# Optimization experiments

Measured on AMD Instinct MI355X. Metric: run time of the kernel, lower is better.

Reference implementation:

```python
import jax, jax.numpy as jnp
import numpy as np
import math

EPS = 1.1920929e-07  # torch default rms_norm eps = finfo(float32).eps

def rms_norm(x):
    return x * jax.lax.rsqrt(jnp.mean(x * x, axis=-1, keepdims=True) + EPS)

def setup_inputs() -> dict:
    key = jax.random.key(0)
    k1, k2, k3, k4 = jax.random.split(key, 4)
    B, T, D = 2, 4096, 2048
    H = 16
    L = (T - 1).bit_length()  # 12
    scale = 0.02
    return {
        "x": jax.random.normal(k1, (B, T, D), dtype=jnp.float32),
        "W_tok": jax.random.normal(k2, (D, D), dtype=jnp.float32) * scale,
        "W_lvl": jax.random.normal(k3, (L * H, D), dtype=jnp.float32) * scale,
        "W_out": jax.random.normal(k4, (D, D), dtype=jnp.float32) * scale,
        "num_heads": H,
    }

def reference(x, W_tok, W_lvl, W_out, num_heads):
    B, T, D = x.shape
    H = num_heads
    Dh = D // H
    L = W_lvl.shape[0] // H  # max_lvls
    inv_sqrt2 = 1.0 / math.sqrt(2.0)

    theta = rms_norm(jnp.einsum('btd,ed->bte', x, W_tok)).reshape(B, T, H, Dh)
    phi = rms_norm(jnp.einsum('btd,ed->bte', x, W_lvl)).reshape(B, T, L, H)

    for l in range(L):  # log-depth butterfly over fixed L levels
        step = 1 << l
        phi_l = phi[:, :, l][..., None]  # [B,T,H,1]
        if step < T:
            theta_prev = jnp.concatenate(
                [jnp.zeros_like(theta[:, :step]), theta[:, :-step]], axis=1)
        else:
            theta_prev = jnp.zeros_like(theta)
        theta = (jnp.cos(phi_l) * theta + jnp.sin(phi_l) * theta_prev) * inv_sqrt2

    y = jnp.einsum('btd,ed->bte', theta.reshape(B, T, D), W_out)
    return y
```

## Files before the change

### kernel.cpp

```cpp
#include <hip/hip_runtime.h>
#include <cstdint>

typedef unsigned short u16;
typedef short bh8 __attribute__((ext_vector_type(8)));
typedef float f32x4 __attribute__((ext_vector_type(4)));

#define EPSF 1.1920929e-07f
#define INV_SQRT2 0.70710678118654752440f

static constexpr size_t OFF_XB   = 0;
static constexpr size_t OFF_WCAT = 33554432;
static constexpr size_t OFF_WOUT = OFF_WCAT + 9437184;
static constexpr size_t OFF_THBF = OFF_WOUT + 8388608;
static constexpr size_t OFF_PHI  = OFF_THBF + 33554432;
static constexpr size_t OFF_TRA  = OFF_PHI + 6291456;
static constexpr size_t OFF_TRB  = OFF_TRA + 6291456;

__device__ __forceinline__ uint32_t f2bf_rne(float f) {
  uint32_t u = __float_as_uint(f);
  u += 0x7fffu + ((u >> 16) & 1u);
  return u >> 16;
}

__device__ __forceinline__ void gload_lds16(const void* g, void* l) {
  __builtin_amdgcn_global_load_lds(
      (const __attribute__((address_space(1))) void*)g,
      (__attribute__((address_space(3))) void*)l, 16, 0, 0);
}

__global__ __launch_bounds__(256)
void cast_f32_bf16(const float* __restrict__ src, u16* __restrict__ dst, int n4) {
  int i = blockIdx.x * blockDim.x + threadIdx.x;
  int stride = gridDim.x * blockDim.x;
  for (; i < n4; i += stride) {
    float4 v = ((const float4*)src)[i];
    uint32_t a = __float_as_uint(v.x); a += 0x7fffu + ((a >> 16) & 1u);
    uint32_t b = __float_as_uint(v.y); b += 0x7fffu + ((b >> 16) & 1u);
    uint32_t c = __float_as_uint(v.z); c += 0x7fffu + ((c >> 16) & 1u);
    uint32_t d = __float_as_uint(v.w); d += 0x7fffu + ((d >> 16) & 1u);
    uint2 o;
    o.x = (a >> 16) | (b & 0xffff0000u);
    o.y = (c >> 16) | (d & 0xffff0000u);
    ((uint2*)dst)[i] = o;
  }
}

__global__ __launch_bounds__(256)
void zero_u16(u16* __restrict__ dst, int n) {
  int i = blockIdx.x * blockDim.x + threadIdx.x;
  int stride = gridDim.x * blockDim.x;
  for (; i < n; i += stride) dst[i] = 0;
}

template<int SPLIT>
__global__ __launch_bounds__(256)
void gemm_bt(const u16* __restrict__ A, const u16* __restrict__ B,
             float* __restrict__ C0, float* __restrict__ C1,
             int K, int ntiles) {
  __shared__ u16 As[128 * 64];
  __shared__ u16 Bs[128 * 64];
  const int tid  = threadIdx.x;
  const int w    = tid >> 6;
  const int lane = tid & 63;
  const int mt = blockIdx.x / ntiles, nt = blockIdx.x % ntiles;
  const int wm = (w >> 1) << 6, wn = (w & 1) << 6;
  const int Kb = K * 2;

  const char* Ab = (const char*)(A + (size_t)mt * 128 * K);
  const char* Bb = (const char*)(B + (size_t)nt * 128 * K);
  char* AsB = (char*)As;
  char* BsB = (char*)Bs;

  const int srow  = w * 8 + (lane >> 3);
  const int scolb = (lane & 7) << 4;

  f32x4 acc[4][4] = {};

  for (int kt = 0; kt < K; kt += 64) {
    #pragma unroll
    for (int i = 0; i < 4; ++i) {
      int row = i * 32 + srow;
      int src = scolb ^ ((row & 7) << 4);
      gload_lds16(Ab + (size_t)row * Kb + kt * 2 + src, AsB + i * 4096 + w * 1024);
      gload_lds16(Bb + (size_t)row * Kb + kt * 2 + src, BsB + i * 4096 + w * 1024);
    }
    __syncthreads();
    #pragma unroll
    for (int kk = 0; kk < 2; ++kk) {
      const int kbyte = kk * 64 + ((lane >> 4) << 4);
      bh8 af[4], bfr[4];
      #pragma unroll
      for (int m = 0; m < 4; ++m) {
        int ar = wm + m * 16 + (lane & 15);
        af[m] = *(const bh8*)(AsB + ar * 128 + (kbyte ^ ((ar & 7) << 4)));
        int br = wn + m * 16 + (lane & 15);
        bfr[m] = *(const bh8*)(BsB + br * 128 + (kbyte ^ ((br & 7) << 4)));
      }
      #pragma unroll
      for (int m = 0; m < 4; ++m)
        #pragma unroll
        for (int n = 0; n < 4; ++n)
          acc[m][n] = __builtin_amdgcn_mfma_f32_16x16x32_bf16(af[m], bfr[n], acc[m][n], 0, 0, 0);
    }
    __syncthreads();
  }

  const int crow0 = mt * 128 + wm + ((lane >> 4) << 2);
  const int ccol0 = nt * 128 + wn + (lane & 15);
  #pragma unroll
  for (int m = 0; m < 4; ++m) {
    #pragma unroll
    for (int n = 0; n < 4; ++n) {
      int gn = ccol0 + n * 16;
      #pragma unroll
      for (int r = 0; r < 4; ++r) {
        int gm = crow0 + m * 16 + r;
        if (SPLIT) {
          if (gn < 2048)      C0[(size_t)gm * 2048 + gn] = acc[m][n][r];
          else if (gn < 2240) C1[(size_t)gm * 192 + (gn - 2048)] = acc[m][n][r];
        } else {
          C0[(size_t)gm * 2048 + gn] = acc[m][n][r];
        }
      }
    }
  }
}

__global__ __launch_bounds__(256)
void rmsnorm_rows(float* __restrict__ th) {
  const int row = blockIdx.x;
  const int tid = threadIdx.x;
  float* p = th + (size_t)row * 2048;
  float4 a = ((const float4*)p)[tid];
  float4 b = ((const float4*)p)[tid + 256];
  float ss = a.x*a.x + a.y*a.y + a.z*a.z + a.w*a.w
           + b.x*b.x + b.y*b.y + b.z*b.z + b.w*b.w;
  #pragma unroll
  for (int o = 32; o > 0; o >>= 1) ss += __shfl_down(ss, o);
  __shared__ float red[4];
  if ((tid & 63) == 0) red[tid >> 6] = ss;
  __syncthreads();
  float tot = red[0] + red[1] + red[2] + red[3];
  float s = rsqrtf(tot * (1.0f / 2048.0f) + EPSF);
  a.x *= s; a.y *= s; a.z *= s; a.w *= s;
  b.x *= s; b.y *= s; b.z *= s; b.w *= s;
  ((float4*)p)[tid] = a;
  ((float4*)p)[tid + 256] = b;
}

__global__ __launch_bounds__(64)
void phi_pass(const float* __restrict__ phiraw,
              float* __restrict__ trigA, float* __restrict__ trigB) {
  const int row = blockIdx.x;
  const int tid = threadIdx.x;
  const float* pr = phiraw + (size_t)row * 192;
  float v0 = pr[tid], v1 = pr[tid + 64], v2 = pr[tid + 128];
  float ss = v0 * v0 + v1 * v1 + v2 * v2;
  #pragma unroll
  for (int o = 32; o > 0; o >>= 1) ss += __shfl_down(ss, o);
  ss = __shfl(ss, 0);
  const float sc = rsqrtf(ss * (1.0f / 192.0f) + EPSF);
  const int b = row >> 12, t = row & 4095;
  const int q = t >> 6, r = t & 63;
  float v[3] = {v0, v1, v2};
  #pragma unroll
  for (int j = 0; j < 3; ++j) {
    int e = j * 64 + tid;
    int l = e >> 4, h = e & 15;
    float ph = v[j] * sc;
    float sn, cs;
    sincosf(ph, &sn, &cs);
    if (l < 6) {
      size_t idx = ((size_t)((b * 16 + h) * 6 + l)) * 4096 + t;
      trigA[idx] = cs; trigA[idx + 786432] = sn;
    } else {
      size_t idx = ((size_t)((b * 16 + h) * 6 + (l - 6))) * 4096 + (size_t)(r * 64 + q);
      trigB[idx] = cs; trigB[idx + 786432] = sn;
    }
  }
}

__global__ __launch_bounds__(512)
void butterflyA(const float* __restrict__ in, u16* __restrict__ outb,
                const float* __restrict__ trigA) {
  __shared__ float L[512 * 32];
  const int tc = blockIdx.x, ec = blockIdx.y, b = blockIdx.z;
  const int tid = threadIdx.x;
  const int t0 = tc * 449;
  const int e0 = ec * 32;
  const int h = e0 >> 7;
  const int pr = tid >> 3;
  const int c4 = (tid & 7) << 2;

  #pragma unroll
  for (int s = 0; s < 8; ++s) {
    int p = pr + s * 64;
    int t = t0 - 63 + p;
    float4 v = make_float4(0.f, 0.f, 0.f, 0.f);
    if (t >= 0 && t < 4096)
      v = *(const float4*)&in[((size_t)(b * 4096 + t)) * 2048 + e0 + c4];
    *(float4*)&L[p * 32 + c4] = v;
  }
  __syncthreads();

  for (int l = 0; l < 6; ++l) {
    const int step = 1 << l;
    const float* cosT = trigA + ((size_t)((b * 16 + h) * 6 + l)) * 4096;
    const float* sinT = cosT + 786432;
    float4 nv[8];
    #pragma unroll
    for (int s = 0; s < 8; ++s) {
      int p = pr + s * 64;
      int t = t0 - 63 + p;
      float4 cur = *(const float4*)&L[p * 32 + c4];
      float4 prev = make_float4(0.f, 0.f, 0.f, 0.f);
      if (p >= step) prev = *(const float4*)&L[(p - step) * 32 + c4];
      float cs = 0.f, sn = 0.f;
      if (t >= 0 && t < 4096) { cs = cosT[t]; sn = sinT[t]; }
      nv[s].x = (cs * cur.x + sn * prev.x) * INV_SQRT2;
      nv[s].y = (cs * cur.y + sn * prev.y) * INV_SQRT2;
      nv[s].z = (cs * cur.z + sn * prev.z) * INV_SQRT2;
      nv[s].w = (cs * cur.w + sn * prev.w) * INV_SQRT2;
    }
    __syncthreads();
    #pragma unroll
    for (int s = 0; s < 8; ++s) {
      int p = pr + s * 64;
      *(float4*)&L[p * 32 + c4] = nv[s];
    }
    __syncthreads();
  }

  #pragma unroll
  for (int s = 0; s < 8; ++s) {
    int p = pr + s * 64;
    int t = t0 - 63 + p;
    if (p >= 63 && t < 4096) {
      float4 v = *(const float4*)&L[p * 32 + c4];
      uint32_t a = f2bf_rne(v.x), bb = f2bf_rne(v.y), c = f2bf_rne(v.z), d = f2bf_rne(v.w);
      uint2 o;
      o.x = a | (bb << 16);
      o.y = c | (d << 16);
      *(uint2*)&outb[((size_t)(b * 4096 + t)) * 2048 + e0 + c4] = o;
    }
  }
}

__global__ __launch_bounds__(256)
void butterflyB(const u16* __restrict__ in, u16* __restrict__ outb,
                const float* __restrict__ trigB) {
  __shared__ float L[64 * 128];
  const int r = blockIdx.x, h = blockIdx.y, b = blockIdx.z;
  const int tid = threadIdx.x;
  const int qr = tid >> 5;
  const int d4 = (tid & 31) << 2;

  #pragma unroll
  for (int s = 0; s < 8; ++s) {
    int q = qr + s * 8;
    int t = q * 64 + r;
    uint2 o = *(const uint2*)&in[((size_t)(b * 4096 + t)) * 2048 + h * 128 + d4];
    float4 v;
    v.x = __uint_as_float((o.x & 0xffffu) << 16);
    v.y = __uint_as_float(o.x & 0xffff0000u);
    v.z = __uint_as_float((o.y & 0xffffu) << 16);
    v.w = __uint_as_float(o.y & 0xffff0000u);
    *(float4*)&L[q * 128 + d4] = v;
  }
  __syncthreads();

  for (int l = 0; l < 6; ++l) {
    const int qs = 1 << l;
    const float* cosT = trigB + ((size_t)((b * 16 + h) * 6 + l)) * 4096 + r * 64;
    const float* sinT = cosT + 786432;
    float4 nv[8];
    #pragma unroll
    for (int s = 0; s < 8; ++s) {
      int q = qr + s * 8;
      float4 cur = *(const float4*)&L[q * 128 + d4];
      float4 prev = make_float4(0.f, 0.f, 0.f, 0.f);
      if (q >= qs) prev = *(const float4*)&L[(q - qs) * 128 + d4];
      float cs = cosT[q], sn = sinT[q];
      nv[s].x = (cs * cur.x + sn * prev.x) * INV_SQRT2;
      nv[s].y = (cs * cur.y + sn * prev.y) * INV_SQRT2;
      nv[s].z = (cs * cur.z + sn * prev.z) * INV_SQRT2;
      nv[s].w = (cs * cur.w + sn * prev.w) * INV_SQRT2;
    }
    __syncthreads();
    #pragma unroll
    for (int s = 0; s < 8; ++s) {
      int q = qr + s * 8;
      *(float4*)&L[q * 128 + d4] = nv[s];
    }
    __syncthreads();
  }

  #pragma unroll
  for (int s = 0; s < 8; ++s) {
    int q = qr + s * 8;
    int t = q * 64 + r;
    float4 v = *(const float4*)&L[q * 128 + d4];
    uint32_t a = f2bf_rne(v.x), bb = f2bf_rne(v.y), c = f2bf_rne(v.z), d = f2bf_rne(v.w);
    uint2 o;
    o.x = a | (bb << 16);
    o.y = c | (d << 16);
    *(uint2*)&outb[((size_t)(b * 4096 + t)) * 2048 + h * 128 + d4] = o;
  }
}

extern "C" void kernel_launch(void* const* d_in, const int* in_sizes, int n_in,
                              void* d_out, int out_size, void* d_ws, size_t ws_size,
                              hipStream_t stream) {
  const float* x    = (const float*)d_in[0];
  const float* Wtok = (const float*)d_in[1];
  const float* Wlvl = (const float*)d_in[2];
  const float* Wout = (const float*)d_in[3];

  char* ws = (char*)d_ws;
  u16*   xb     = (u16*)(ws + OFF_XB);
  u16*   wcat   = (u16*)(ws + OFF_WCAT);
  u16*   woutb  = (u16*)(ws + OFF_WOUT);
  u16*   thbfA  = (u16*)(ws + OFF_XB);
  u16*   thbfB  = (u16*)(ws + OFF_THBF);
  float* phiraw = (float*)(ws + OFF_PHI);
  float* trigA  = (float*)(ws + OFF_TRA);
  float* trigB  = (float*)(ws + OFF_TRB);
  float* out    = (float*)d_out;

  cast_f32_bf16<<<2048, 256, 0, stream>>>(x, xb, 4194304);
  cast_f32_bf16<<<1024, 256, 0, stream>>>(Wtok, wcat, 1048576);
  cast_f32_bf16<<<384, 256, 0, stream>>>(Wlvl, wcat + (size_t)2048 * 2048, 98304);
  zero_u16<<<128, 256, 0, stream>>>(wcat + (size_t)2240 * 2048, 131072);
  cast_f32_bf16<<<1024, 256, 0, stream>>>(Wout, woutb, 1048576);

  gemm_bt<1><<<64 * 18, 256, 0, stream>>>(xb, wcat, out, phiraw, 2048, 18);

  rmsnorm_rows<<<8192, 256, 0, stream>>>(out);

  phi_pass<<<8192, 64, 0, stream>>>(phiraw, trigA, trigB);

  butterflyA<<<dim3(10, 64, 2), 512, 0, stream>>>(out, thbfA, trigA);

  butterflyB<<<dim3(64, 16, 2), 256, 0, stream>>>(thbfA, thbfB, trigB);

  gemm_bt<0><<<64 * 16, 256, 0, stream>>>(thbfB, woutb, out, nullptr, 2048, 16);
}
```

Baseline: 461.9 us.

## Replace GEMMs with 256x256 triple-buffered kernel, fuse rmsnorm into epilogue, split-K phi

Replaces the 128x128 GEMM with a 256x256-tile, 512-thread kernel that triple-buffers LDS loads, raises MFMA priority and remaps workgroups in XCD-aware order. The first GEMM computes per-row sum-of-squares via atomics, so the separate rmsnorm pass is dropped and the scaling is applied when the butterfly loads. The small phi projection is computed as split-K tiles whose partials are summed in phi_pass, which now uses fast __sinf/__cosf and one unified trig layout. The aim is less memory traffic and better MFMA utilization, at the cost of atomics, reduced trig precision and greater register/LDS pressure.

```diff
diff --git a/kernel.cpp b/kernel.cpp
--- a/kernel.cpp
+++ b/kernel.cpp
@@ -7,14 +7,14 @@
 
 #define EPSF 1.1920929e-07f
 #define INV_SQRT2 0.70710678118654752440f
+#define SINOFF 1572864
 
 static constexpr size_t OFF_XB   = 0;
 static constexpr size_t OFF_WCAT = 33554432;
 static constexpr size_t OFF_WOUT = OFF_WCAT + 9437184;
 static constexpr size_t OFF_THBF = OFF_WOUT + 8388608;
-static constexpr size_t OFF_PHI  = OFF_THBF + 33554432;
-static constexpr size_t OFF_TRA  = OFF_PHI + 6291456;
-static constexpr size_t OFF_TRB  = OFF_TRA + 6291456;
+static constexpr size_t OFF_TRIG = OFF_THBF + 33554432;
+static constexpr size_t OFF_SSQ  = OFF_TRIG + 12582912;
 
 __device__ __forceinline__ uint32_t f2bf_rne(float f) {
   uint32_t u = __float_as_uint(f);
@@ -26,6 +26,12 @@
   __builtin_amdgcn_global_load_lds(
       (const __attribute__((address_space(1))) void*)g,
       (__attribute__((address_space(3))) void*)l, 16, 0, 0);
+}
+
+__global__ __launch_bounds__(256)
+void zero_f32(float4* __restrict__ p, int n4) {
+  int i = blockIdx.x * blockDim.x + threadIdx.x;
+  if (i < n4) p[i] = make_float4(0.f, 0.f, 0.f, 0.f);
 }
 
 __global__ __launch_bounds__(256)
@@ -45,144 +51,166 @@
   }
 }
 
-__global__ __launch_bounds__(256)
-void zero_u16(u16* __restrict__ dst, int n) {
-  int i = blockIdx.x * blockDim.x + threadIdx.x;
-  int stride = gridDim.x * blockDim.x;
-  for (; i < n; i += stride) dst[i] = 0;
-}
-
-template<int SPLIT>
-__global__ __launch_bounds__(256)
-void gemm_bt(const u16* __restrict__ A, const u16* __restrict__ B,
-             float* __restrict__ C0, float* __restrict__ C1,
-             int K, int ntiles) {
-  __shared__ u16 As[128 * 64];
-  __shared__ u16 Bs[128 * 64];
+template<int MODE>
+__global__ __launch_bounds__(512, 2)
+void gemm8(const u16* __restrict__ A, const u16* __restrict__ B,
+           float* __restrict__ C, float* __restrict__ phiq,
+           float* __restrict__ sumsq, int nwg) {
+  __shared__ __align__(16) char ldsb[98304];
   const int tid  = threadIdx.x;
   const int w    = tid >> 6;
   const int lane = tid & 63;
-  const int mt = blockIdx.x / ntiles, nt = blockIdx.x % ntiles;
-  const int wm = (w >> 1) << 6, wn = (w & 1) << 6;
-  const int Kb = K * 2;
-
-  const char* Ab = (const char*)(A + (size_t)mt * 128 * K);
-  const char* Bb = (const char*)(B + (size_t)nt * 128 * K);
-  char* AsB = (char*)As;
-  char* BsB = (char*)Bs;
-
-  const int srow  = w * 8 + (lane >> 3);
-  const int scolb = (lane & 7) << 4;
-
-  f32x4 acc[4][4] = {};
-
-  for (int kt = 0; kt < K; kt += 64) {
-    #pragma unroll
-    for (int i = 0; i < 4; ++i) {
-      int row = i * 32 + srow;
-      int src = scolb ^ ((row & 7) << 4);
-      gload_lds16(Ab + (size_t)row * Kb + kt * 2 + src, AsB + i * 4096 + w * 1024);
-      gload_lds16(Bb + (size_t)row * Kb + kt * 2 + src, BsB + i * 4096 + w * 1024);
-    }
-    __syncthreads();
-    #pragma unroll
-    for (int kk = 0; kk < 2; ++kk) {
-      const int kbyte = kk * 64 + ((lane >> 4) << 4);
-      bh8 af[4], bfr[4];
+  const int cpx = nwg >> 3;
+  const int wg  = ((int)blockIdx.x & 7) * cpx + ((int)blockIdx.x >> 3);
+
+  int mt, nt, t0, TT, kq = 0;
+  bool isphi = false;
+  if (MODE == 0) { mt = wg >> 3; nt = wg & 7; t0 = 0; TT = 64; }
+  else {
+    if (wg < 256) { mt = wg >> 3; nt = wg & 7; t0 = 0; TT = 64; }
+    else { int idx = wg - 256; mt = idx >> 2; kq = idx & 3; nt = 8; t0 = kq * 16; TT = 16; isphi = true; }
+  }
+  const int wr = w >> 2, wc = w & 3;
+
+  const char* Ab = (const char*)A + (size_t)mt * 256 * 4096;
+  const char* Bb = (const char*)B + (size_t)nt * 256 * 4096;
+
+  const int row0 = ((tid >> 6) << 4) + (tid & 15);
+  const int g16  = ((tid >> 4) & 3) << 4;
+  const char* sA0 = Ab + (size_t)row0 * 4096 + g16 + (size_t)t0 * 64;
+  const char* sA1 = sA0 + 128 * 4096;
+  const char* sB0 = Bb + (size_t)row0 * 4096 + g16 + (size_t)t0 * 64;
+  const char* sB1 = sB0 + 128 * 4096;
+  const int wB = w * 1024;
+  const int lo16 = lane * 16;
+
+  f32x4 acc[8][4] = {};
+
+#define STG(tt, cb) do { \
+    gload_lds16(sA0 + (tt) * 64, ldsb + (cb) * 32768 + wB); \
+    gload_lds16(sA1 + (tt) * 64, ldsb + (cb) * 32768 + 8192 + wB); \
+    gload_lds16(sB0 + (tt) * 64, ldsb + (cb) * 32768 + 16384 + wB); \
+    gload_lds16(sB1 + (tt) * 64, ldsb + (cb) * 32768 + 24576 + wB); } while (0)
+
+  STG(0, 0);
+  STG(1, 1);
+  asm volatile("s_waitcnt vmcnt(4)" ::: "memory");
+  __builtin_amdgcn_s_barrier();
+
+  int c = 0;
+  for (int t = 0; t < TT; ++t) {
+    int c2 = c + 2; if (c2 >= 3) c2 -= 3;
+    if (t + 2 < TT) STG(t + 2, c2);
+    const char* A_ = ldsb + c * 32768 + wr * 8192;
+    const char* B_ = ldsb + c * 32768 + 16384 + wc * 4096;
+    bh8 bf[4], af[8];
+    #pragma unroll
+    for (int n = 0; n < 4; ++n) bf[n] = *(const bh8*)(B_ + n * 1024 + lo16);
+    #pragma unroll
+    for (int m = 0; m < 8; ++m) af[m] = *(const bh8*)(A_ + m * 1024 + lo16);
+    __builtin_amdgcn_s_setprio(1);
+    #pragma unroll
+    for (int m = 0; m < 8; ++m)
       #pragma unroll
-      for (int m = 0; m < 4; ++m) {
-        int ar = wm + m * 16 + (lane & 15);
-        af[m] = *(const bh8*)(AsB + ar * 128 + (kbyte ^ ((ar & 7) << 4)));
-        int br = wn + m * 16 + (lane & 15);
-        bfr[m] = *(const bh8*)(BsB + br * 128 + (kbyte ^ ((br & 7) << 4)));
+      for (int n = 0; n < 4; ++n)
+        acc[m][n] = __builtin_amdgcn_mfma_f32_16x16x32_bf16(af[m], bf[n], acc[m][n], 0, 0, 0);
+    __builtin_amdgcn_s_setprio(0);
+    if (t + 1 < TT) {
+      if (t + 2 < TT) asm volatile("s_waitcnt vmcnt(4)" ::: "memory");
+      else            asm volatile("s_waitcnt vmcnt(0)" ::: "memory");
+      __builtin_amdgcn_s_barrier();
+      c = (c == 2) ? 0 : c + 1;
+    }
+  }
+#undef STG
+
+  const int crow = (lane >> 4) << 2;
+  const int ccol = lane & 15;
+
+  if (MODE == 1 && isphi) {
+    #pragma unroll
+    for (int m = 0; m < 8; ++m) {
+      int gm = mt * 256 + wr * 128 + m * 16 + crow;
+      #pragma unroll
+      for (int n = 0; n < 4; ++n) {
+        int gn = wc * 64 + n * 16 + ccol;
+        if (gn < 192) {
+          #pragma unroll
+          for (int r = 0; r < 4; ++r)
+            phiq[(size_t)kq * SINOFF + (size_t)(gm + r) * 192 + gn] = acc[m][n][r];
+        }
       }
+    }
+    return;
+  }
+
+  #pragma unroll
+  for (int m = 0; m < 8; ++m) {
+    int gm = mt * 256 + wr * 128 + m * 16 + crow;
+    #pragma unroll
+    for (int n = 0; n < 4; ++n) {
+      int gn = nt * 256 + wc * 64 + n * 16 + ccol;
       #pragma unroll
-      for (int m = 0; m < 4; ++m)
-        #pragma unroll
-        for (int n = 0; n < 4; ++n)
-          acc[m][n] = __builtin_amdgcn_mfma_f32_16x16x32_bf16(af[m], bfr[n], acc[m][n], 0, 0, 0);
-    }
-    __syncthreads();
-  }
-
-  const int crow0 = mt * 128 + wm + ((lane >> 4) << 2);
-  const int ccol0 = nt * 128 + wn + (lane & 15);
-  #pragma unroll
-  for (int m = 0; m < 4; ++m) {
-    #pragma unroll
-    for (int n = 0; n < 4; ++n) {
-      int gn = ccol0 + n * 16;
+      for (int r = 0; r < 4; ++r)
+        C[(size_t)(gm + r) * 2048 + gn] = acc[m][n][r];
+    }
+  }
+
+  if (MODE == 1) {
+    __syncthreads();
+    float* red = (float*)ldsb;
+    #pragma unroll
+    for (int m = 0; m < 8; ++m)
       #pragma unroll
       for (int r = 0; r < 4; ++r) {
-        int gm = crow0 + m * 16 + r;
-        if (SPLIT) {
-          if (gn < 2048)      C0[(size_t)gm * 2048 + gn] = acc[m][n][r];
-          else if (gn < 2240) C1[(size_t)gm * 192 + (gn - 2048)] = acc[m][n][r];
-        } else {
-          C0[(size_t)gm * 2048 + gn] = acc[m][n][r];
-        }
+        float s = 0.f;
+        #pragma unroll
+        for (int n = 0; n < 4; ++n) { float v = acc[m][n][r]; s += v * v; }
+        s += __shfl_xor(s, 1); s += __shfl_xor(s, 2);
+        s += __shfl_xor(s, 4); s += __shfl_xor(s, 8);
+        if ((lane & 15) == 0)
+          red[(wr * 128 + m * 16 + crow + r) * 4 + wc] = s;
       }
-    }
-  }
-}
-
-__global__ __launch_bounds__(256)
-void rmsnorm_rows(float* __restrict__ th) {
+    __syncthreads();
+    if (tid < 256) {
+      float s = red[tid * 4] + red[tid * 4 + 1] + red[tid * 4 + 2] + red[tid * 4 + 3];
+      atomicAdd(&sumsq[mt * 256 + tid], s);
+    }
+  }
+}
+
+__global__ __launch_bounds__(64)
+void phi_pass(const float* __restrict__ phiq, float* __restrict__ trig) {
   const int row = blockIdx.x;
   const int tid = threadIdx.x;
-  float* p = th + (size_t)row * 2048;
-  float4 a = ((const float4*)p)[tid];
-  float4 b = ((const float4*)p)[tid + 256];
-  float ss = a.x*a.x + a.y*a.y + a.z*a.z + a.w*a.w
-           + b.x*b.x + b.y*b.y + b.z*b.z + b.w*b.w;
-  #pragma unroll
-  for (int o = 32; o > 0; o >>= 1) ss += __shfl_down(ss, o);
-  __shared__ float red[4];
-  if ((tid & 63) == 0) red[tid >> 6] = ss;
-  __syncthreads();
-  float tot = red[0] + red[1] + red[2] + red[3];
-  float s = rsqrtf(tot * (1.0f / 2048.0f) + EPSF);
-  a.x *= s; a.y *= s; a.z *= s; a.w *= s;
-  b.x *= s; b.y *= s; b.z *= s; b.w *= s;
-  ((float4*)p)[tid] = a;
-  ((float4*)p)[tid + 256] = b;
-}
-
-__global__ __launch_bounds__(64)
-void phi_pass(const float* __restrict__ phiraw,
-              float* __restrict__ trigA, float* __restrict__ trigB) {
-  const int row = blockIdx.x;
-  const int tid = threadIdx.x;
-  const float* pr = phiraw + (size_t)row * 192;
-  float v0 = pr[tid], v1 = pr[tid + 64], v2 = pr[tid + 128];
+  const float* p0 = phiq + (size_t)row * 192;
+  float v0 = 0.f, v1 = 0.f, v2 = 0.f;
+  #pragma unroll
+  for (int kq = 0; kq < 4; ++kq) {
+    const float* p = p0 + (size_t)kq * SINOFF;
+    v0 += p[tid]; v1 += p[tid + 64]; v2 += p[tid + 128];
+  }
   float ss = v0 * v0 + v1 * v1 + v2 * v2;
   #pragma unroll
   for (int o = 32; o > 0; o >>= 1) ss += __shfl_down(ss, o);
   ss = __shfl(ss, 0);
   const float sc = rsqrtf(ss * (1.0f / 192.0f) + EPSF);
   const int b = row >> 12, t = row & 4095;
-  const int q = t >> 6, r = t & 63;
   float v[3] = {v0, v1, v2};
   #pragma unroll
   for (int j = 0; j < 3; ++j) {
     int e = j * 64 + tid;
     int l = e >> 4, h = e & 15;
     float ph = v[j] * sc;
-    float sn, cs;
-    sincosf(ph, &sn, &cs);
-    if (l < 6) {
-      size_t idx = ((size_t)((b * 16 + h) * 6 + l)) * 4096 + t;
-      trigA[idx] = cs; trigA[idx + 786432] = sn;
-    } else {
-      size_t idx = ((size_t)((b * 16 + h) * 6 + (l - 6))) * 4096 + (size_t)(r * 64 + q);
-      trigB[idx] = cs; trigB[idx + 786432] = sn;
-    }
+    float cs = __cosf(ph), sn = __sinf(ph);
+    size_t idx = ((size_t)((b * 16 + h) * 12 + l)) * 4096 + t;
+    trig[idx] = cs; trig[idx + SINOFF] = sn;
   }
 }
 
 __global__ __launch_bounds__(512)
 void butterflyA(const float* __restrict__ in, u16* __restrict__ outb,
-                const float* __restrict__ trigA) {
+                const float* __restrict__ trig, const float* __restrict__ sumsq) {
   __shared__ float L[512 * 32];
   const int tc = blockIdx.x, ec = blockIdx.y, b = blockIdx.z;
   const int tid = threadIdx.x;
@@ -197,16 +225,18 @@
     int p = pr + s * 64;
     int t = t0 - 63 + p;
     float4 v = make_float4(0.f, 0.f, 0.f, 0.f);
-    if (t >= 0 && t < 4096)
+    if (t >= 0 && t < 4096) {
       v = *(const float4*)&in[((size_t)(b * 4096 + t)) * 2048 + e0 + c4];
+      float scl = rsqrtf(sumsq[b * 4096 + t] * (1.0f / 2048.0f) + EPSF);
+      v.x *= scl; v.y *= scl; v.z *= scl; v.w *= scl;
+    }
     *(float4*)&L[p * 32 + c4] = v;
   }
   __syncthreads();
 
   for (int l = 0; l < 6; ++l) {
     const int step = 1 << l;
-    const float* cosT = trigA + ((size_t)((b * 16 + h) * 6 + l)) * 4096;
-    const float* sinT = cosT + 786432;
+    const float* cosT = trig + ((size_t)((b * 16 + h) * 12 + l)) * 4096;
     float4 nv[8];
     #pragma unroll
     for (int s = 0; s < 8; ++s) {
@@ -216,7 +246,7 @@
       float4 prev = make_float4(0.f, 0.f, 0.f, 0.f);
       if (p >= step) prev = *(const float4*)&L[(p - step) * 32 + c4];
       float cs = 0.f, sn = 0.f;
-      if (t >= 0 && t < 4096) { cs = cosT[t]; sn = sinT[t]; }
+      if (t >= 0 && t < 4096) { cs = cosT[t]; sn = cosT[SINOFF + t]; }
       nv[s].x = (cs * cur.x + sn * prev.x) * INV_SQRT2;
       nv[s].y = (cs * cur.y + sn * prev.y) * INV_SQRT2;
       nv[s].z = (cs * cur.z + sn * prev.z) * INV_SQRT2;
@@ -248,7 +278,7 @@
 
 __global__ __launch_bounds__(256)
 void butterflyB(const u16* __restrict__ in, u16* __restrict__ outb,
-                const float* __restrict__ trigB) {
+                const float* __restrict__ trig) {
   __shared__ float L[64 * 128];
   const int r = blockIdx.x, h = blockIdx.y, b = blockIdx.z;
   const int tid = threadIdx.x;
@@ -271,8 +301,7 @@
 
   for (int l = 0; l < 6; ++l) {
     const int qs = 1 << l;
-    const float* cosT = trigB + ((size_t)((b * 16 + h) * 6 + l)) * 4096 + r * 64;
-    const float* sinT = cosT + 786432;
+    const float* cosT = trig + ((size_t)((b * 16 + h) * 12 + 6 + l)) * 4096 + r;
     float4 nv[8];
     #pragma unroll
     for (int s = 0; s < 8; ++s) {
@@ -280,7 +309,7 @@
       float4 cur = *(const float4*)&L[q * 128 + d4];
       float4 prev = make_float4(0.f, 0.f, 0.f, 0.f);
       if (q >= qs) prev = *(const float4*)&L[(q - qs) * 128 + d4];
-      float cs = cosT[q], sn = sinT[q];
+      float cs = cosT[q << 6], sn = cosT[SINOFF + (q << 6)];
       nv[s].x = (cs * cur.x + sn * prev.x) * INV_SQRT2;
       nv[s].y = (cs * cur.y + sn * prev.y) * INV_SQRT2;
       nv[s].z = (cs * cur.z + sn * prev.z) * INV_SQRT2;
@@ -320,28 +349,27 @@
   u16*   xb     = (u16*)(ws + OFF_XB);
   u16*   wcat   = (u16*)(ws + OFF_WCAT);
   u16*   woutb  = (u16*)(ws + OFF_WOUT);
-  u16*   thbfA  = (u16*)(ws + OFF_XB);
-  u16*   thbfB  = (u16*)(ws + OFF_THBF);
-  float* phiraw = (float*)(ws + OFF_PHI);
-  float* trigA  = (float*)(ws + OFF_TRA);
-  float* trigB  = (float*)(ws + OFF_TRB);
+  u16*   thA    = (u16*)(ws + OFF_XB);
+  u16*   thB    = (u16*)(ws + OFF_THBF);
+  float* phiq   = (float*)(ws + OFF_THBF);
+  float* trig   = (float*)(ws + OFF_TRIG);
+  float* sumsq  = (float*)(ws + OFF_SSQ);
   float* out    = (float*)d_out;
+
+  zero_f32<<<8, 256, 0, stream>>>((float4*)sumsq, 2048);
 
   cast_f32_bf16<<<2048, 256, 0, stream>>>(x, xb, 4194304);
   cast_f32_bf16<<<1024, 256, 0, stream>>>(Wtok, wcat, 1048576);
   cast_f32_bf16<<<384, 256, 0, stream>>>(Wlvl, wcat + (size_t)2048 * 2048, 98304);
-  zero_u16<<<128, 256, 0, stream>>>(wcat + (size_t)2240 * 2048, 131072);
   cast_f32_bf16<<<1024, 256, 0, stream>>>(Wout, woutb, 1048576);
 
-  gemm_bt<1><<<64 * 18, 256, 0, stream>>>(xb, wcat, out, phiraw, 2048, 18);
-
-  rmsnorm_rows<<<8192, 256, 0, stream>>>(out);
-
-  phi_pass<<<8192, 64, 0, stream>>>(phiraw, trigA, trigB);
-
-  butterflyA<<<dim3(10, 64, 2), 512, 0, stream>>>(out, thbfA, trigA);
-
-  butterflyB<<<dim3(64, 16, 2), 256, 0, stream>>>(thbfA, thbfB, trigB);
-
-  gemm_bt<0><<<64 * 16, 256, 0, stream>>>(thbfB, woutb, out, nullptr, 2048, 16);
-}
+  gemm8<1><<<384, 512, 0, stream>>>(xb, wcat, out, phiq, sumsq, 384);
+
+  phi_pass<<<8192, 64, 0, stream>>>(phiq, trig);
+
+  butterflyA<<<dim3(10, 64, 2), 512, 0, stream>>>(out, thA, trig, sumsq);
+
+  butterflyB<<<dim3(64, 16, 2), 256, 0, stream>>>(thA, thB, trig);
+
+  gemm8<0><<<256, 512, 0, stream>>>(thB, woutb, out, nullptr, nullptr, 256);
+}
```

After: 461.6 us. No clear change (-0.1%).

## Add 256x256 pipelined output GEMM and fuse RMS scaling into butterfly

Applied to the files above, without the earlier changes.

Replaces the final output GEMM with a new 256x256-tile, 512-thread kernel. It double-buffers its LDS loads via direct global-to-LDS copies, interleaves them with MFMA phases, raises wave priority around the MFMAs, and remaps workgroups across XCDs. The rmsnorm pass now writes only per-row scales, which butterflyA applies on load, removing a full read-write pass over theta. It also merges the two trig tables into a single layout, swaps sincosf for fast __sinf/__cosf, and drops the zero-fill kernel for the padded weight rows. Risks include lower accuracy from the fast trig intrinsics, strided trig reads in butterflyB, and the padded weight region possibly holding stale data, though its columns are discarded.

```diff
diff --git a/kernel.cpp b/kernel.cpp
--- a/kernel.cpp
+++ b/kernel.cpp
@@ -7,14 +7,15 @@
 
 #define EPSF 1.1920929e-07f
 #define INV_SQRT2 0.70710678118654752440f
+#define SINOFF 1572864
 
 static constexpr size_t OFF_XB   = 0;
 static constexpr size_t OFF_WCAT = 33554432;
+static constexpr size_t OFF_SC   = OFF_WCAT + 9175040;
 static constexpr size_t OFF_WOUT = OFF_WCAT + 9437184;
 static constexpr size_t OFF_THBF = OFF_WOUT + 8388608;
 static constexpr size_t OFF_PHI  = OFF_THBF + 33554432;
-static constexpr size_t OFF_TRA  = OFF_PHI + 6291456;
-static constexpr size_t OFF_TRB  = OFF_TRA + 6291456;
+static constexpr size_t OFF_TRIG = OFF_PHI + 6291456;
 
 __device__ __forceinline__ uint32_t f2bf_rne(float f) {
   uint32_t u = __float_as_uint(f);
@@ -45,13 +46,6 @@
   }
 }
 
-__global__ __launch_bounds__(256)
-void zero_u16(u16* __restrict__ dst, int n) {
-  int i = blockIdx.x * blockDim.x + threadIdx.x;
-  int stride = gridDim.x * blockDim.x;
-  for (; i < n; i += stride) dst[i] = 0;
-}
-
 template<int SPLIT>
 __global__ __launch_bounds__(256)
 void gemm_bt(const u16* __restrict__ A, const u16* __restrict__ B,
@@ -126,11 +120,143 @@
   }
 }
 
+__global__ __launch_bounds__(512, 1)
+void gemm256(const u16* __restrict__ A, const u16* __restrict__ B,
+             float* __restrict__ C, int ntiles, int nwg) {
+  __shared__ __align__(16) char lds[131072];
+  const int tid = threadIdx.x;
+  const int w = tid >> 6, lane = tid & 63;
+  const int wr = w >> 2, wc = w & 3;
+  const int cpx = nwg >> 3;
+  const int wg = ((int)blockIdx.x & 7) * cpx + ((int)blockIdx.x >> 3);
+  const int mt = wg / ntiles, nt = wg % ntiles;
+
+  const char* Ab = (const char*)A + (size_t)mt * 256 * 4096;
+  const char* Bb = (const char*)B + (size_t)nt * 256 * 4096;
+  const char* pA = Ab + (lane & 15) * 4096 + (lane >> 4) * 16 + (size_t)w * 16 * 4096;
+  const char* pB = Bb + (lane & 15) * 4096 + (lane >> 4) * 16 + (size_t)w * 16 * 4096;
+  char* ldsA = lds;
+  char* ldsB = lds + 65536;
+  const int wst = w * 2048;
+  const int lo16 = lane * 16;
+
+#define STGA(tt, h, b) do { \
+    gload_lds16(pA + (h) * 524288 + (tt) * 128,      ldsA + (b) * 32768 + (h) * 16384 + wst); \
+    gload_lds16(pA + (h) * 524288 + (tt) * 128 + 64, ldsA + (b) * 32768 + (h) * 16384 + wst + 1024); } while (0)
+#define STGB(tt, h, b) do { \
+    gload_lds16(pB + (h) * 524288 + (tt) * 128,      ldsB + (b) * 32768 + (h) * 16384 + wst); \
+    gload_lds16(pB + (h) * 524288 + (tt) * 128 + 64, ldsB + (b) * 32768 + (h) * 16384 + wst + 1024); } while (0)
+
+  f32x4 acc[8][4] = {};
+  bh8 amlo[4][2], amhi[4][2], bnlo[2][2], bnhi[2][2];
+
+  STGA(0, 0, 0); STGA(0, 1, 0); STGB(0, 0, 0); STGB(0, 1, 0);
+  STGA(1, 0, 1); STGA(1, 1, 1);
+  asm volatile("s_waitcnt vmcnt(4)" ::: "memory");
+  __builtin_amdgcn_s_barrier();
+
+  for (int t = 0; t < 32; ++t) {
+    const int c = t & 1, d = c ^ 1;
+    const char* Abase = ldsA + c * 32768 + wr * 16384;
+    const char* Bbase = ldsB + c * 32768 + wc * 8192;
+
+    #pragma unroll
+    for (int m = 0; m < 4; ++m)
+      #pragma unroll
+      for (int kk = 0; kk < 2; ++kk)
+        amlo[m][kk] = *(const bh8*)(Abase + m * 2048 + kk * 1024 + lo16);
+    #pragma unroll
+    for (int n = 0; n < 2; ++n)
+      #pragma unroll
+      for (int kk = 0; kk < 2; ++kk)
+        bnlo[n][kk] = *(const bh8*)(Bbase + n * 2048 + kk * 1024 + lo16);
+    if (t + 1 < 32) STGB(t + 1, 0, d);
+    __builtin_amdgcn_s_barrier();
+    __builtin_amdgcn_s_setprio(1);
+    #pragma unroll
+    for (int m = 0; m < 4; ++m)
+      #pragma unroll
+      for (int n = 0; n < 2; ++n)
+        #pragma unroll
+        for (int kk = 0; kk < 2; ++kk)
+          acc[m][n] = __builtin_amdgcn_mfma_f32_16x16x32_bf16(amlo[m][kk], bnlo[n][kk], acc[m][n], 0, 0, 0);
+    __builtin_amdgcn_s_setprio(0);
+    __builtin_amdgcn_s_barrier();
+
+    #pragma unroll
+    for (int m = 0; m < 4; ++m)
+      #pragma unroll
+      for (int kk = 0; kk < 2; ++kk)
+        amhi[m][kk] = *(const bh8*)(Abase + (m + 4) * 2048 + kk * 1024 + lo16);
+    if (t + 1 < 32) STGB(t + 1, 1, d);
+    __builtin_amdgcn_s_barrier();
+    __builtin_amdgcn_s_setprio(1);
+    #pragma unroll
+    for (int m = 0; m < 4; ++m)
+      #pragma unroll
+      for (int n = 0; n < 2; ++n)
+        #pragma unroll
+        for (int kk = 0; kk < 2; ++kk)
+          acc[m + 4][n] = __builtin_amdgcn_mfma_f32_16x16x32_bf16(amhi[m][kk], bnlo[n][kk], acc[m + 4][n], 0, 0, 0);
+    __builtin_amdgcn_s_setprio(0);
+    __builtin_amdgcn_s_barrier();
+
+    #pragma unroll
+    for (int n = 0; n < 2; ++n)
+      #pragma unroll
+      for (int kk = 0; kk < 2; ++kk)
+        bnhi[n][kk] = *(const bh8*)(Bbase + (n + 2) * 2048 + kk * 1024 + lo16);
+    if (t + 2 < 32) STGA(t + 2, 0, c);
+    __builtin_amdgcn_s_barrier();
+    __builtin_amdgcn_s_setprio(1);
+    #pragma unroll
+    for (int m = 0; m < 4; ++m)
+      #pragma unroll
+      for (int n = 0; n < 2; ++n)
+        #pragma unroll
+        for (int kk = 0; kk < 2; ++kk)
+          acc[m + 4][n + 2] = __builtin_amdgcn_mfma_f32_16x16x32_bf16(amhi[m][kk], bnhi[n][kk], acc[m + 4][n + 2], 0, 0, 0);
+    __builtin_amdgcn_s_setprio(0);
+    __builtin_amdgcn_s_barrier();
+
+    if (t + 2 < 32) STGA(t + 2, 1, c);
+    __builtin_amdgcn_s_barrier();
+    __builtin_amdgcn_s_setprio(1);
+    #pragma unroll
+    for (int m = 0; m < 4; ++m)
+      #pragma unroll
+      for (int n = 0; n < 2; ++n)
+        #pragma unroll
+        for (int kk = 0; kk < 2; ++kk)
+          acc[m][n + 2] = __builtin_amdgcn_mfma_f32_16x16x32_bf16(amlo[m][kk], bnhi[n][kk], acc[m][n + 2], 0, 0, 0);
+    __builtin_amdgcn_s_setprio(0);
+    if (t < 30) asm volatile("s_waitcnt vmcnt(4)" ::: "memory");
+    else        asm volatile("s_waitcnt vmcnt(0)" ::: "memory");
+    __builtin_amdgcn_s_barrier();
+  }
+#undef STGA
+#undef STGB
+
+  const int crow = (lane >> 4) << 2;
+  const int ccol = lane & 15;
+  #pragma unroll
+  for (int m = 0; m < 8; ++m) {
+    int gm = mt * 256 + wr * 128 + m * 16 + crow;
+    #pragma unroll
+    for (int n = 0; n < 4; ++n) {
+      int gn = nt * 256 + wc * 64 + n * 16 + ccol;
+      #pragma unroll
+      for (int r = 0; r < 4; ++r)
+        C[(size_t)(gm + r) * 2048 + gn] = acc[m][n][r];
+    }
+  }
+}
+
 __global__ __launch_bounds__(256)
-void rmsnorm_rows(float* __restrict__ th) {
+void rmsnorm_scales(const float* __restrict__ th, float* __restrict__ sc) {
   const int row = blockIdx.x;
   const int tid = threadIdx.x;
-  float* p = th + (size_t)row * 2048;
+  const float* p = th + (size_t)row * 2048;
   float4 a = ((const float4*)p)[tid];
   float4 b = ((const float4*)p)[tid + 256];
   float ss = a.x*a.x + a.y*a.y + a.z*a.z + a.w*a.w
@@ -140,17 +266,14 @@
   __shared__ float red[4];
   if ((tid & 63) == 0) red[tid >> 6] = ss;
   __syncthreads();
-  float tot = red[0] + red[1] + red[2] + red[3];
-  float s = rsqrtf(tot * (1.0f / 2048.0f) + EPSF);
-  a.x *= s; a.y *= s; a.z *= s; a.w *= s;
-  b.x *= s; b.y *= s; b.z *= s; b.w *= s;
-  ((float4*)p)[tid] = a;
-  ((float4*)p)[tid + 256] = b;
+  if (tid == 0) {
+    float tot = red[0] + red[1] + red[2] + red[3];
+    sc[row] = rsqrtf(tot * (1.0f / 2048.0f) + EPSF);
+  }
 }
 
 __global__ __launch_bounds__(64)
-void phi_pass(const float* __restrict__ phiraw,
-              float* __restrict__ trigA, float* __restrict__ trigB) {
+void phi_pass(const float* __restrict__ phiraw, float* __restrict__ trig) {
   const int row = blockIdx.x;
   const int tid = threadIdx.x;
   const float* pr = phiraw + (size_t)row * 192;
@@ -161,28 +284,21 @@
   ss = __shfl(ss, 0);
   const float sc = rsqrtf(ss * (1.0f / 192.0f) + EPSF);
   const int b = row >> 12, t = row & 4095;
-  const int q = t >> 6, r = t & 63;
   float v[3] = {v0, v1, v2};
   #pragma unroll
   for (int j = 0; j < 3; ++j) {
     int e = j * 64 + tid;
     int l = e >> 4, h = e & 15;
     float ph = v[j] * sc;
-    float sn, cs;
-    sincosf(ph, &sn, &cs);
-    if (l < 6) {
-      size_t idx = ((size_t)((b * 16 + h) * 6 + l)) * 4096 + t;
-      trigA[idx] = cs; trigA[idx + 786432] = sn;
-    } else {
-      size_t idx = ((size_t)((b * 16 + h) * 6 + (l - 6))) * 4096 + (size_t)(r * 64 + q);
-      trigB[idx] = cs; trigB[idx + 786432] = sn;
-    }
+    float cs = __cosf(ph), sn = __sinf(ph);
+    size_t idx = ((size_t)((b * 16 + h) * 12 + l)) * 4096 + t;
+    trig[idx] = cs; trig[idx + SINOFF] = sn;
   }
 }
 
 __global__ __launch_bounds__(512)
 void butterflyA(const float* __restrict__ in, u16* __restrict__ outb,
-                const float* __restrict__ trigA) {
+                const float* __restrict__ trig, const float* __restrict__ scales) {
   __shared__ float L[512 * 32];
   const int tc = blockIdx.x, ec = blockIdx.y, b = blockIdx.z;
   const int tid = threadIdx.x;
@@ -197,16 +313,18 @@
     int p = pr + s * 64;
     int t = t0 - 63 + p;
     float4 v = make_float4(0.f, 0.f, 0.f, 0.f);
-    if (t >= 0 && t < 4096)
+    if (t >= 0 && t < 4096) {
       v = *(const float4*)&in[((size_t)(b * 4096 + t)) * 2048 + e0 + c4];
+      float scl = scales[b * 4096 + t];
+      v.x *= scl; v.y *= scl; v.z *= scl; v.w *= scl;
+    }
     *(float4*)&L[p * 32 + c4] = v;
   }
   __syncthreads();
 
   for (int l = 0; l < 6; ++l) {
     const int step = 1 << l;
-    const float* cosT = trigA + ((size_t)((b * 16 + h) * 6 + l)) * 4096;
-    const float* sinT = cosT + 786432;
+    const float* cosT = trig + ((size_t)((b * 16 + h) * 12 + l)) * 4096;
     float4 nv[8];
     #pragma unroll
     for (int s = 0; s < 8; ++s) {
@@ -216,7 +334,7 @@
       float4 prev = make_float4(0.f, 0.f, 0.f, 0.f);
       if (p >= step) prev = *(const float4*)&L[(p - step) * 32 + c4];
       float cs = 0.f, sn = 0.f;
-      if (t >= 0 && t < 4096) { cs = cosT[t]; sn = sinT[t]; }
+      if (t >= 0 && t < 4096) { cs = cosT[t]; sn = cosT[SINOFF + t]; }
       nv[s].x = (cs * cur.x + sn * prev.x) * INV_SQRT2;
       nv[s].y = (cs * cur.y + sn * prev.y) * INV_SQRT2;
       nv[s].z = (cs * cur.z + sn * prev.z) * INV_SQRT2;
@@ -248,7 +366,7 @@
 
 __global__ __launch_bounds__(256)
 void butterflyB(const u16* __restrict__ in, u16* __restrict__ outb,
-                const float* __restrict__ trigB) {
+                const float* __restrict__ trig) {
   __shared__ float L[64 * 128];
   const int r = blockIdx.x, h = blockIdx.y, b = blockIdx.z;
   const int tid = threadIdx.x;
@@ -271,8 +389,7 @@
 
   for (int l = 0; l < 6; ++l) {
     const int qs = 1 << l;
-    const float* cosT = trigB + ((size_t)((b * 16 + h) * 6 + l)) * 4096 + r * 64;
-    const float* sinT = cosT + 786432;
+    const float* cosT = trig + ((size_t)((b * 16 + h) * 12 + 6 + l)) * 4096 + r;
     float4 nv[8];
     #pragma unroll
     for (int s = 0; s < 8; ++s) {
@@ -280,7 +397,7 @@
       float4 cur = *(const float4*)&L[q * 128 + d4];
       float4 prev = make_float4(0.f, 0.f, 0.f, 0.f);
       if (q >= qs) prev = *(const float4*)&L[(q - qs) * 128 + d4];
-      float cs = cosT[q], sn = sinT[q];
+      float cs = cosT[q << 6], sn = cosT[SINOFF + (q << 6)];
       nv[s].x = (cs * cur.x + sn * prev.x) * INV_SQRT2;
       nv[s].y = (cs * cur.y + sn * prev.y) * INV_SQRT2;
       nv[s].z = (cs * cur.z + sn * prev.z) * INV_SQRT2;
@@ -320,28 +437,27 @@
   u16*   xb     = (u16*)(ws + OFF_XB);
   u16*   wcat   = (u16*)(ws + OFF_WCAT);
   u16*   woutb  = (u16*)(ws + OFF_WOUT);
-  u16*   thbfA  = (u16*)(ws + OFF_XB);
-  u16*   thbfB  = (u16*)(ws + OFF_THBF);
+  u16*   thA    = (u16*)(ws + OFF_XB);
+  u16*   thB    = (u16*)(ws + OFF_THBF);
+  float* scales = (float*)(ws + OFF_SC);
   float* phiraw = (float*)(ws + OFF_PHI);
-  float* trigA  = (float*)(ws + OFF_TRA);
-  float* trigB  = (float*)(ws + OFF_TRB);
+  float* trig   = (float*)(ws + OFF_TRIG);
   float* out    = (float*)d_out;
 
   cast_f32_bf16<<<2048, 256, 0, stream>>>(x, xb, 4194304);
   cast_f32_bf16<<<1024, 256, 0, stream>>>(Wtok, wcat, 1048576);
   cast_f32_bf16<<<384, 256, 0, stream>>>(Wlvl, wcat + (size_t)2048 * 2048, 98304);
-  zero_u16<<<128, 256, 0, stream>>>(wcat + (size_t)2240 * 2048, 131072);
   cast_f32_bf16<<<1024, 256, 0, stream>>>(Wout, woutb, 1048576);
 
   gemm_bt<1><<<64 * 18, 256, 0, stream>>>(xb, wcat, out, phiraw, 2048, 18);
 
-  rmsnorm_rows<<<8192, 256, 0, stream>>>(out);
-
-  phi_pass<<<8192, 64, 0, stream>>>(phiraw, trigA, trigB);
-
-  butterflyA<<<dim3(10, 64, 2), 512, 0, stream>>>(out, thbfA, trigA);
-
-  butterflyB<<<dim3(64, 16, 2), 256, 0, stream>>>(thbfA, thbfB, trigB);
-
-  gemm_bt<0><<<64 * 16, 256, 0, stream>>>(thbfB, woutb, out, nullptr, 2048, 16);
-}
+  rmsnorm_scales<<<8192, 256, 0, stream>>>(out, scales);
+
+  phi_pass<<<8192, 64, 0, stream>>>(phiraw, trig);
+
+  butterflyA<<<dim3(10, 64, 2), 512, 0, stream>>>(out, thA, trig, scales);
+
+  butterflyB<<<dim3(64, 16, 2), 256, 0, stream>>>(thA, thB, trig);
+
+  gemm256<<<256, 512, 0, stream>>>(thB, woutb, out, 8, 256);
+}
```

After: 441.7 us. -4.4%, faster.
